# Kernel tuning notes

Hardware: AMD Instinct MI355X
Metric: run time of the kernel (lower is better)

Reference implementation:

```python
import jax, jax.numpy as jnp
import numpy as np

D_MODEL = 512
NUM_HEADS = 8
HEAD_DIM = D_MODEL // NUM_HEADS  # 64
EMBEDDING_DIM = 512  # undefined global EmbeddingDim in source -> d_model
EVENT_DIM = 388      # undefined global EventDim in source -> MIDI event vocab
B, T = 2, 2048


def setup_inputs() -> dict:
    key = jax.random.key(0)
    ks = jax.random.split(key, 12)
    sc = 0.02
    v = jax.random.normal(ks[0], (B, T, D_MODEL), jnp.float32)
    k = jax.random.normal(ks[1], (B, T, D_MODEL), jnp.float32)
    q = jax.random.normal(ks[2], (B, T, D_MODEL), jnp.float32)
    mask = jnp.tril(jnp.ones((T, T), jnp.float32))  # causal mask, broadcasts to [H,B,T,T]
    Wq = jax.random.normal(ks[3], (D_MODEL, HEAD_DIM), jnp.float32) * sc
    bq = jnp.zeros((HEAD_DIM,), jnp.float32)
    Wk = jax.random.normal(ks[4], (D_MODEL, HEAD_DIM), jnp.float32) * sc
    bk = jnp.zeros((HEAD_DIM,), jnp.float32)
    Wv = jax.random.normal(ks[5], (D_MODEL, HEAD_DIM), jnp.float32) * sc
    bv = jnp.zeros((HEAD_DIM,), jnp.float32)
    E = jax.random.normal(ks[6], (NUM_HEADS, T, HEAD_DIM), jnp.float32) * sc
    Wo = jax.random.normal(ks[7], (D_MODEL, EMBEDDING_DIM), jnp.float32) * sc
    bo = jnp.zeros((EMBEDDING_DIM,), jnp.float32)
    Wl = jax.random.normal(ks[8], (EMBEDDING_DIM, EVENT_DIM), jnp.float32) * sc
    bl = jnp.zeros((EVENT_DIM,), jnp.float32)
    return {"v": v, "k": k, "q": q, "mask": mask, "Wq": Wq, "bq": bq,
            "Wk": Wk, "bk": bk, "Wv": Wv, "bv": bv, "E": E,
            "Wo": Wo, "bo": bo, "Wl": Wl, "bl": bl}


def _skew(S):
    # S: [H,B,T,T] -> Music-Transformer skew via left-pad, reshape, slice
    H, Bb, Tt, _ = S.shape
    S = jnp.pad(S, ((0, 0), (0, 0), (0, 0), (1, 0)))          # [H,B,T,T+1]
    S = S.reshape(H, Bb, Tt + 1, Tt)                           # [H,B,T+1,T]
    return S[:, :, 1:]                                         # [H,B,T,T]


def reference(v, k, q, mask, Wq, bq, Wk, bk, Wv, bv, E, Wo, bo, Wl, bl):
    # The source applies the SAME Dense per head, so all heads share q/k/v projections
    qh = q @ Wq + bq  # [B,T,hd]
    kh = k @ Wk + bk  # [B,T,hd]
    vh = v @ Wv + bv  # [B,T,hd]
    # relative-position scores per head: Q @ E^T then skew
    S = jnp.einsum('btd,hsd->hbts', qh, E)  # [H,B,T,T]
    S = _skew(S)
    qk = jnp.einsum('btd,bsd->bts', qh, kh)  # [B,T,T], identical across heads
    attn = (qk[None] + S) / np.sqrt(HEAD_DIM)  # [H,B,T,T]
    attn = attn * mask - jnp.asarray(1e10, attn.dtype) * (1.0 - mask)
    score = jax.nn.softmax(attn, axis=-1)
    ctx = jnp.einsum('hbts,bsd->hbtd', score, vh)  # [H,B,T,hd]
    ctx = jnp.transpose(ctx, (1, 2, 0, 3)).reshape(ctx.shape[1], ctx.shape[2], -1)  # [B,T,d_model]
    ctx = jax.nn.relu(ctx @ Wo + bo)  # [B,T,EmbeddingDim]
    logits = ctx @ Wl + bl            # [B,T,EventDim]
    return logits
```

## Files before the change

kernel.cpp:

```cpp
#include <hip/hip_runtime.h>
#include <hip/hip_bf16.h>


#define B_ 2
#define T_ 2048
#define DM_ 512
#define H_ 8
#define HD_ 64
#define ED_ 512
#define EV_ 388
#define BT_ (B_ * T_)

typedef __attribute__((ext_vector_type(8))) short short8;
typedef __attribute__((ext_vector_type(4))) float floatx4;

#define MFMA(a, b, c) __builtin_amdgcn_mfma_f32_16x16x32_bf16((a), (b), (c), 0, 0, 0)

__device__ __forceinline__ float bfs(unsigned short s) {
  union { unsigned int i; float f; } v; v.i = ((unsigned int)s) << 16; return v.f;
}
__device__ __forceinline__ unsigned short f2bf(float f) {
  __hip_bfloat16 h = __float2bfloat16(f);
  union { __hip_bfloat16 h; unsigned short u; } v; v.h = h; return v.u;
}
__device__ __forceinline__ float ldf(const void* p, int i, bool isbf) {
  return isbf ? bfs(((const unsigned short*)p)[i]) : ((const float*)p)[i];
}
__device__ __forceinline__ bool det_bf(const unsigned int* mask) {
  return mask[0] != 0x3F800000u;
}
__device__ __forceinline__ void gl_lds16(const unsigned short* g, void* l) {
  __builtin_amdgcn_global_load_lds(
      (const __attribute__((address_space(1))) void*)g,
      (__attribute__((address_space(3))) void*)l, 16, 0, 0);
}

__global__ __launch_bounds__(256) void prep_kernel(
    const void* __restrict__ E, const void* __restrict__ Wq,
    const void* __restrict__ Wk, const void* __restrict__ Wv,
    const void* __restrict__ Wo, const void* __restrict__ Wl,
    const unsigned int* __restrict__ mask,
    unsigned short* __restrict__ E_c, unsigned short* __restrict__ WqT,
    unsigned short* __restrict__ WkT, unsigned short* __restrict__ WvT,
    unsigned short* __restrict__ WoT, unsigned short* __restrict__ WlT) {
  const bool isbf = det_bf(mask);
  const int tid = threadIdx.x;
  int bi = blockIdx.x;
  if (bi < 1024) {
    const int i0 = (bi * 256 + tid) * 4;
    if (isbf) {
      *(uint2*)&E_c[i0] = *(const uint2*)((const unsigned short*)E + i0);
    } else {
      float4 f = *(const float4*)((const float*)E + i0);
      unsigned short p[4] = {f2bf(f.x), f2bf(f.y), f2bf(f.z), f2bf(f.w)};
      *(uint2*)&E_c[i0] = *(uint2*)p;
    }
    return;
  }
  bi -= 1024;
  const void* src; unsigned short* dst; int N, nb;
  if (bi < 16)       { src = Wq; dst = WqT; N = 64;  nb = bi; }
  else if (bi < 32)  { src = Wk; dst = WkT; N = 64;  nb = bi - 16; }
  else if (bi < 48)  { src = Wv; dst = WvT; N = 64;  nb = bi - 32; }
  else if (bi < 176) { src = Wo; dst = WoT; N = 512; nb = bi - 48; }
  else               { src = Wl; dst = WlT; N = 388; nb = bi - 176; }
  const int n = nb * 4 + (tid >> 6);
  const int k0 = (tid & 63) * 8;
  unsigned short vv[8];
#pragma unroll
  for (int j = 0; j < 8; ++j) {
    if (n >= N) vv[j] = 0;
    else if (isbf) vv[j] = ((const unsigned short*)src)[(size_t)(k0 + j) * N + n];
    else vv[j] = f2bf(((const float*)src)[(size_t)(k0 + j) * N + n]);
  }
  *(uint4*)&dst[(size_t)n * DM_ + k0] = *(uint4*)vv;
}

__global__ __launch_bounds__(256) void gemm_proj(
    const void* __restrict__ xq, const void* __restrict__ xk,
    const void* __restrict__ xv,
    const unsigned short* __restrict__ WqT, const unsigned short* __restrict__ WkT,
    const unsigned short* __restrict__ WvT,
    const void* __restrict__ bq, const void* __restrict__ bk,
    const void* __restrict__ bv, const unsigned int* __restrict__ mask,
    unsigned short* __restrict__ oq, unsigned short* __restrict__ ok,
    unsigned short* __restrict__ ovt) {
  __shared__ __align__(16) short sA[64][72];
  __shared__ __align__(16) short sW[64][72];
  const int sel = blockIdx.y;
  const void* x = (sel == 0) ? xq : (sel == 1) ? xk : xv;
  const unsigned short* WT = (sel == 0) ? WqT : (sel == 1) ? WkT : WvT;
  const void* bias = (sel == 0) ? bq : (sel == 1) ? bk : bv;
  const bool isbf = det_bf(mask);

  const int tid = threadIdx.x;
  const int w = tid >> 6, lane = tid & 63;
  const int q_ = lane >> 4, n_ = lane & 15;
  const int row0 = blockIdx.x * 64;

  floatx4 acc[4];
#pragma unroll
  for (int j = 0; j < 4; ++j) acc[j] = (floatx4){0.f, 0.f, 0.f, 0.f};

  for (int k0 = 0; k0 < DM_; k0 += 64) {
    if (isbf) {
#pragma unroll
      for (int it = 0; it < 2; ++it) {
        int idx = tid + it * 256;
        int rr = idx >> 3, cc = (idx & 7) * 8;
        *(uint4*)&sA[rr][cc] =
            *(const uint4*)((const unsigned short*)x + (size_t)(row0 + rr) * DM_ + k0 + cc);
      }
    } else {
#pragma unroll
      for (int it = 0; it < 4; ++it) {
        int idx = tid + it * 256;
        int rr = idx >> 4, cc = (idx & 15) * 4;
        float4 f = *(const float4*)((const float*)x + (size_t)(row0 + rr) * DM_ + k0 + cc);
        unsigned short p[4] = {f2bf(f.x), f2bf(f.y), f2bf(f.z), f2bf(f.w)};
        *(uint2*)&sA[rr][cc] = *(uint2*)p;
      }
    }
#pragma unroll
    for (int it = 0; it < 2; ++it) {
      int idx = tid + it * 256;
      int rr = idx >> 3, cc = (idx & 7) * 8;
      *(uint4*)&sW[rr][cc] = *(const uint4*)(WT + (size_t)rr * DM_ + k0 + cc);
    }
    __syncthreads();
    short8 a0 = *(const short8*)&sA[16 * w + n_][8 * q_];
    short8 a1 = *(const short8*)&sA[16 * w + n_][32 + 8 * q_];
#pragma unroll
    for (int nb = 0; nb < 4; ++nb) {
      short8 b0 = *(const short8*)&sW[16 * nb + n_][8 * q_];
      short8 b1 = *(const short8*)&sW[16 * nb + n_][32 + 8 * q_];
      acc[nb] = MFMA(a0, b0, acc[nb]);
      acc[nb] = MFMA(a1, b1, acc[nb]);
    }
    __syncthreads();
  }

#pragma unroll
  for (int nb = 0; nb < 4; ++nb) {
    const int col = 16 * nb + n_;
    const float bb = ldf(bias, col, isbf);
#pragma unroll
    for (int r = 0; r < 4; ++r) {
      int row = row0 + 16 * w + 4 * q_ + r;
      unsigned short val = f2bf(acc[nb][r] + bb);
      if (sel < 2) {
        unsigned short* o = (sel == 0) ? oq : ok;
        o[(size_t)row * HD_ + col] = val;
      } else {
        int b = row >> 11, s = row & 2047;
        ovt[(((size_t)(b * HD_ + col)) << 11) + s] = val;
      }
    }
  }
}

__device__ __forceinline__ int pbase_of(int ti) {
  return (ti < 22) ? (ti - 11) * 2 : 22 + (ti - 22) * 3;
}

__global__ __launch_bounds__(256, 4) void attn_kernel(
    const unsigned short* __restrict__ qh, const unsigned short* __restrict__ kh,
    const unsigned short* __restrict__ vt, const unsigned short* __restrict__ E,
    unsigned short* __restrict__ ctxo, float* __restrict__ pc,
    float* __restrict__ ml) {
  __shared__ __align__(16) short sK[2][64][64];
  __shared__ __align__(16) short sVT[2][64][64];
  __shared__ __align__(16) short sP[64][64];

  const int id = blockIdx.x;
  const int hb = id / 63;
  const int rem = id % 63;
  int ti, c, nc;
  if (rem < 11)      { ti = rem;                  c = 0;              nc = 1; }
  else if (rem < 33) { ti = 11 + ((rem - 11) >> 1); c = (rem - 11) & 1; nc = 2; }
  else               { ti = 22 + (rem - 33) / 3;    c = (rem - 33) % 3; nc = 3; }
  const int nsteps = ti + 1;
  const int klo = (c * nsteps) / nc;
  const int khi = ((c + 1) * nsteps) / nc;

  const int h = hb >> 1, b = hb & 1;
  const int t0 = ti * 64;

  const int tid = threadIdx.x;
  const int w = tid >> 6, lane = tid & 63;
  const int q_ = lane >> 4, n_ = lane & 15;

  const int trow = t0 + 16 * w + n_;
  const unsigned short* qp = qh + (((size_t)((b << 11) + trow)) << 6) + (q_ << 3);
  const short8 qa0 = *(const short8*)qp;
  const short8 qa1 = *(const short8*)(qp + 32);

  short8 onesf;
#pragma unroll
  for (int j = 0; j < 8; ++j) onesf[j] = (short)0x3F80;

  floatx4 ctxa[4];
#pragma unroll
  for (int nb = 0; nb < 4; ++nb) ctxa[nb] = (floatx4){0.f, 0.f, 0.f, 0.f};
  floatx4 lacc = (floatx4){0.f, 0.f, 0.f, 0.f};

  const unsigned short* eb = E + ((size_t)h << 17);
  const unsigned short* kbase = kh + (((size_t)(b << 11)) << 6);
  const unsigned short* vbase = vt + (((size_t)(b << 6)) << 11);

  const int lrow = lane >> 3;
  const int lchunk = ((lane & 7) ^ lrow) << 3;
  const int rK0 = 8 * w + lrow;
  const int c0s = ((q_ ^ (n_ & 7)) << 3);
  const int c1s = (((q_ | 4) ^ (n_ & 7)) << 3);

#define STAGE(bufsel, s0v)                                                     \
  {                                                                            \
    void* dK = (void*)&sK[bufsel][8 * w][0];                                   \
    void* dV = (void*)&sVT[bufsel][8 * w][0];                                  \
    const unsigned short* gK =                                                 \
        kbase + (((size_t)((s0v) + rK0)) << 6) + lchunk;                       \
    const unsigned short* gV =                                                 \
        vbase + (((size_t)rK0) << 11) + (s0v) + lchunk;                        \
    gl_lds16(gK, dK);                                                          \
    gl_lds16(gK + (32 << 6), (void*)((short*)dK + 32 * 64));                   \
    gl_lds16(gV, dV);                                                          \
    gl_lds16(gV + (32 << 11), (void*)((short*)dV + 32 * 64));                  \
  }

  STAGE(0, klo * 64);

  for (int kt = klo; kt < khi; ++kt) {
    const int cur = (kt - klo) & 1;
    const int s0 = kt * 64;

    asm volatile("s_waitcnt vmcnt(0)" ::: "memory");
    __builtin_amdgcn_sched_barrier(0);
    __builtin_amdgcn_s_barrier();
    __builtin_amdgcn_sched_barrier(0);

    if (kt + 1 < khi) STAGE(cur ^ 1, s0 + 64);

    const int rb = (T_ - 64) + s0 - t0;
    short8 e0[5], e1[5];
#pragma unroll
    for (int f = 0; f < 5; ++f) {
      int gr = rb + 16 * (3 - w + f) + n_;
      if (gr > T_ - 1) gr = T_ - 1;
      const unsigned short* ep = eb + ((size_t)gr << 6) + (q_ << 3);
      e0[f] = *(const short8*)ep;
      e1[f] = *(const short8*)(ep + 32);
    }

    floatx4 qk[4];
    __builtin_amdgcn_s_setprio(1);
#pragma unroll
    for (int nb = 0; nb < 4; ++nb) {
      short8 kb0 = *(const short8*)&sK[cur][16 * nb + n_][c0s];
      short8 kb1 = *(const short8*)&sK[cur][16 * nb + n_][c1s];
      qk[nb] = (floatx4){0.f, 0.f, 0.f, 0.f};
      qk[nb] = MFMA(qa0, kb0, qk[nb]);
      qk[nb] = MFMA(qa1, kb1, qk[nb]);
    }
    floatx4 qe[5];
#pragma unroll
    for (int f = 0; f < 5; ++f) {
      qe[f] = (floatx4){0.f, 0.f, 0.f, 0.f};
      qe[f] = MFMA(qa0, e0[f], qe[f]);
      qe[f] = MFMA(qa1, e1[f], qe[f]);
    }
    __builtin_amdgcn_s_setprio(0);

    const bool diag = (kt == ti);
#pragma unroll
    for (int r = 0; r < 4; ++r) {
      const int t = 4 * q_ + r;
      const int ba = ((q_ << 4) | ((n_ - t + 15) & 15)) << 2;
      const int nd = (n_ + t + 1) & 15;
      const bool hi = nd > t;
      const int swr = (t & 7) << 3;
#pragma unroll
      for (int mb = 0; mb < 4; ++mb) {
        float merged = hi ? qe[mb + 1][r] : qe[mb][r];
        float g = __int_as_float(
            __builtin_amdgcn_ds_bpermute(ba, __float_as_int(merged)));
        float sv = qk[mb][r] + g;
        if (diag && (16 * mb + n_ > 16 * w + t)) sv = -1.0e30f;
        sP[16 * w + t][(16 * mb + n_) ^ swr] =
            (short)f2bf(exp2f(sv * 0.18033688011f));
      }
    }

    short8 pa0 = *(const short8*)&sP[16 * w + n_][c0s];
    short8 pa1 = *(const short8*)&sP[16 * w + n_][c1s];
    __builtin_amdgcn_s_setprio(1);
#pragma unroll
    for (int nb = 0; nb < 4; ++nb) {
      short8 v0 = *(const short8*)&sVT[cur][16 * nb + n_][c0s];
      short8 v1 = *(const short8*)&sVT[cur][16 * nb + n_][c1s];
      ctxa[nb] = MFMA(pa0, v0, ctxa[nb]);
      ctxa[nb] = MFMA(pa1, v1, ctxa[nb]);
    }
    lacc = MFMA(pa0, onesf, lacc);
    lacc = MFMA(pa1, onesf, lacc);
    __builtin_amdgcn_s_setprio(0);
  }
#undef STAGE

  if (nc == 1) {
#pragma unroll
    for (int r = 0; r < 4; ++r) {
      const float inv = 1.0f / lacc[r];
      const int row = t0 + 16 * w + 4 * q_ + r;
      const size_t base = (((size_t)((b << 11) + row)) << 9) + (h << 6) + n_;
#pragma unroll
      for (int nb = 0; nb < 4; ++nb)
        ctxo[base + 16 * nb] = f2bf(ctxa[nb][r] * inv);
    }
  } else {
    const int idx = hb * 52 + pbase_of(ti) + c;
    float* pcb = pc + ((size_t)idx << 12);
    float* mlb = ml + ((size_t)idx << 6);
#pragma unroll
    for (int r = 0; r < 4; ++r) {
      const int row = 16 * w + 4 * q_ + r;
#pragma unroll
      for (int nb = 0; nb < 4; ++nb)
        pcb[(row << 6) + 16 * nb + n_] = ctxa[nb][r];
      if (n_ == 0) mlb[row] = lacc[r];
    }
  }
}

__global__ __launch_bounds__(256) void combine_kernel(
    const float* __restrict__ pc, const float* __restrict__ ml,
    unsigned short* __restrict__ ctxo) {
  const int cb = blockIdx.x;
  const int hb = cb / 21;
  const int ti = 11 + cb % 21;
  const int nc = (ti < 22) ? 2 : 3;
  const int h = hb >> 1, b = hb & 1, t0 = ti * 64;
  const int tid = threadIdx.x;
  const int row = tid >> 2, seg = (tid & 3) * 16;
  const int idx0 = hb * 52 + pbase_of(ti);

  float lsum = 0.f;
  float4 a4[4];
#pragma unroll
  for (int j = 0; j < 4; ++j) a4[j] = (float4){0.f, 0.f, 0.f, 0.f};
  for (int c = 0; c < nc; ++c) {
    const int idx = idx0 + c;
    lsum += ml[((size_t)idx << 6) + row];
    const float* cp = pc + ((size_t)idx << 12) + (row << 6) + seg;
#pragma unroll
    for (int j = 0; j < 4; ++j) {
      float4 x = *(const float4*)(cp + 4 * j);
      a4[j].x += x.x; a4[j].y += x.y; a4[j].z += x.z; a4[j].w += x.w;
    }
  }
  const float inv = 1.0f / lsum;
  unsigned short o[16];
#pragma unroll
  for (int j = 0; j < 4; ++j) {
    o[4 * j + 0] = f2bf(a4[j].x * inv);
    o[4 * j + 1] = f2bf(a4[j].y * inv);
    o[4 * j + 2] = f2bf(a4[j].z * inv);
    o[4 * j + 3] = f2bf(a4[j].w * inv);
  }
  unsigned short* dst =
      ctxo + (((size_t)((b << 11) + t0 + row)) << 9) + (h << 6) + seg;
  *(uint4*)dst = *(uint4*)&o[0];
  *(uint4*)(dst + 8) = *(uint4*)&o[8];
}

template <int RELU>
__global__ __launch_bounds__(256) void mlp_mfma(
    const unsigned short* __restrict__ A, const unsigned short* __restrict__ WT,
    const void* __restrict__ bias, unsigned short* __restrict__ outBF,
    void* __restrict__ outD, const unsigned int* __restrict__ mask) {
  __shared__ __align__(16) short sA[64][72];
  __shared__ __align__(16) short sW[64][72];
  const int tid = threadIdx.x;
  const int w = tid >> 6, lane = tid & 63;
  const int q_ = lane >> 4, n_ = lane & 15;
  const int row0 = blockIdx.x * 64;
  const int n0 = blockIdx.y * 64;
  const bool isbf = det_bf(mask);

  floatx4 acc[4];
#pragma unroll
  for (int j = 0; j < 4; ++j) acc[j] = (floatx4){0.f, 0.f, 0.f, 0.f};

  for (int k0 = 0; k0 < DM_; k0 += 64) {
#pragma unroll
    for (int it = 0; it < 2; ++it) {
      int idx = tid + it * 256;
      int rr = idx >> 3, cc = (idx & 7) * 8;
      *(uint4*)&sA[rr][cc] = *(const uint4*)(A + (size_t)(row0 + rr) * DM_ + k0 + cc);
      *(uint4*)&sW[rr][cc] = *(const uint4*)(WT + (size_t)(n0 + rr) * DM_ + k0 + cc);
    }
    __syncthreads();
    short8 a0 = *(const short8*)&sA[16 * w + n_][8 * q_];
    short8 a1 = *(const short8*)&sA[16 * w + n_][32 + 8 * q_];
#pragma unroll
    for (int nb = 0; nb < 4; ++nb) {
      short8 b0 = *(const short8*)&sW[16 * nb + n_][8 * q_];
      short8 b1 = *(const short8*)&sW[16 * nb + n_][32 + 8 * q_];
      acc[nb] = MFMA(a0, b0, acc[nb]);
      acc[nb] = MFMA(a1, b1, acc[nb]);
    }
    __syncthreads();
  }

#pragma unroll
  for (int nb = 0; nb < 4; ++nb) {
    const int col = n0 + 16 * nb + n_;
    float bb = 0.f;
    if (RELU || col < EV_) bb = ldf(bias, col, isbf);
#pragma unroll
    for (int r = 0; r < 4; ++r) {
      const int row = row0 + 16 * w + 4 * q_ + r;
      float v = acc[nb][r] + bb;
      if (RELU) {
        outBF[(size_t)row * ED_ + col] = f2bf(fmaxf(v, 0.f));
      } else if (col < EV_) {
        if (isbf) ((unsigned short*)outD)[(size_t)row * EV_ + col] = f2bf(v);
        else      ((float*)outD)[(size_t)row * EV_ + col] = v;
      }
    }
  }
}

extern "C" void kernel_launch(void* const* d_in, const int* in_sizes, int n_in,
                              void* d_out, int out_size, void* d_ws, size_t ws_size,
                              hipStream_t stream) {
  const void* v  = d_in[0];
  const void* k  = d_in[1];
  const void* q  = d_in[2];
  const unsigned int* mask = (const unsigned int*)d_in[3];
  const void* Wq = d_in[4];
  const void* bq = d_in[5];
  const void* Wk = d_in[6];
  const void* bk = d_in[7];
  const void* Wv = d_in[8];
  const void* bv = d_in[9];
  const void* E  = d_in[10];
  const void* Wo = d_in[11];
  const void* bo = d_in[12];
  const void* Wl = d_in[13];
  const void* bl = d_in[14];

  char* p = (char*)d_ws;
  unsigned short* E_c  = (unsigned short*)p; p += (size_t)H_ * T_ * HD_ * 2;
  unsigned short* qhb  = (unsigned short*)p; p += (size_t)BT_ * HD_ * 2;
  unsigned short* khb  = (unsigned short*)p; p += (size_t)BT_ * HD_ * 2;
  unsigned short* vtb  = (unsigned short*)p; p += (size_t)BT_ * HD_ * 2;
  unsigned short* WqT  = (unsigned short*)p; p += (size_t)HD_ * DM_ * 2;
  unsigned short* WkT  = (unsigned short*)p; p += (size_t)HD_ * DM_ * 2;
  unsigned short* WvT  = (unsigned short*)p; p += (size_t)HD_ * DM_ * 2;
  unsigned short* WoT  = (unsigned short*)p; p += (size_t)ED_ * DM_ * 2;
  unsigned short* WlT  = (unsigned short*)p; p += (size_t)448 * DM_ * 2;
  unsigned short* ctxb = (unsigned short*)p; p += (size_t)BT_ * DM_ * 2;
  unsigned short* h1b  = (unsigned short*)p; p += (size_t)BT_ * ED_ * 2;
  float* pc = (float*)p; p += (size_t)16 * 52 * 4096 * 4;
  float* ml = (float*)p; p += (size_t)16 * 52 * 64 * 4;

  prep_kernel<<<dim3(1312), 256, 0, stream>>>(
      E, Wq, Wk, Wv, Wo, Wl, mask, E_c, WqT, WkT, WvT, WoT, WlT);
  gemm_proj<<<dim3(BT_ / 64, 3), 256, 0, stream>>>(
      q, k, v, WqT, WkT, WvT, bq, bk, bv, mask, qhb, khb, vtb);
  attn_kernel<<<dim3(1008), 256, 0, stream>>>(qhb, khb, vtb, E_c, ctxb, pc, ml);
  combine_kernel<<<dim3(336), 256, 0, stream>>>(pc, ml, ctxb);
  mlp_mfma<1><<<dim3(BT_ / 64, ED_ / 64), 256, 0, stream>>>(
      ctxb, WoT, bo, h1b, nullptr, mask);
  mlp_mfma<0><<<dim3(BT_ / 64, 448 / 64), 256, 0, stream>>>(
      h1b, WlT, bl, nullptr, d_out, mask);
}
```

Measured before the change: 217.9 us.

## Halve attention KV tile to 32 and split causal rows into more chunks

After: 310.4 us. +42.4%, slower.

```diff
diff --git a/kernel.cpp b/kernel.cpp
--- a/kernel.cpp
+++ b/kernel.cpp
@@ -160,26 +160,33 @@
 }
 
 __device__ __forceinline__ int pbase_of(int ti) {
-  return (ti < 22) ? (ti - 11) * 2 : 22 + (ti - 22) * 3;
-}
-
-__global__ __launch_bounds__(256, 4) void attn_kernel(
+  return (ti < 11) ? (ti - 5) * 2
+       : (ti < 16) ? 12 + (ti - 11) * 3
+       : (ti < 22) ? 27 + (ti - 16) * 4
+       : (ti < 27) ? 51 + (ti - 22) * 5
+                   : 76 + (ti - 27) * 6;
+}
+
+__global__ __launch_bounds__(256, 8) void attn_kernel(
     const unsigned short* __restrict__ qh, const unsigned short* __restrict__ kh,
     const unsigned short* __restrict__ vt, const unsigned short* __restrict__ E,
     unsigned short* __restrict__ ctxo, float* __restrict__ pc,
     float* __restrict__ ml) {
-  __shared__ __align__(16) short sK[2][64][64];
-  __shared__ __align__(16) short sVT[2][64][64];
-  __shared__ __align__(16) short sP[64][64];
+  __shared__ __align__(16) short sK[2][32][64];
+  __shared__ __align__(16) short sVT[2][64][32];
+  __shared__ __align__(16) short sP[64][32];
 
   const int id = blockIdx.x;
-  const int hb = id / 63;
-  const int rem = id % 63;
+  const int hb = id / 111;
+  const int rem = id % 111;
   int ti, c, nc;
-  if (rem < 11)      { ti = rem;                  c = 0;              nc = 1; }
-  else if (rem < 33) { ti = 11 + ((rem - 11) >> 1); c = (rem - 11) & 1; nc = 2; }
-  else               { ti = 22 + (rem - 33) / 3;    c = (rem - 33) % 3; nc = 3; }
-  const int nsteps = ti + 1;
+  if (rem < 5)       { ti = rem;                  c = 0;              nc = 1; }
+  else if (rem < 17) { ti = 5 + (rem - 5) / 2;    c = (rem - 5) % 2;  nc = 2; }
+  else if (rem < 32) { ti = 11 + (rem - 17) / 3;  c = (rem - 17) % 3; nc = 3; }
+  else if (rem < 56) { ti = 16 + (rem - 32) / 4;  c = (rem - 32) % 4; nc = 4; }
+  else if (rem < 81) { ti = 22 + (rem - 56) / 5;  c = (rem - 56) % 5; nc = 5; }
+  else               { ti = 27 + (rem - 81) / 6;  c = (rem - 81) % 6; nc = 6; }
+  const int nsteps = 2 * (ti + 1);
   const int klo = (c * nsteps) / nc;
   const int khi = ((c + 1) * nsteps) / nc;
 
@@ -208,101 +215,96 @@
   const unsigned short* kbase = kh + (((size_t)(b << 11)) << 6);
   const unsigned short* vbase = vt + (((size_t)(b << 6)) << 11);
 
-  const int lrow = lane >> 3;
-  const int lchunk = ((lane & 7) ^ lrow) << 3;
-  const int rK0 = 8 * w + lrow;
+  const int kRow = lane >> 3;
+  const int kChk = ((lane & 7) ^ kRow) << 3;
+  const int vRow = lane >> 2;
+  const int vChk = ((lane & 3) ^ (vRow & 3)) << 3;
   const int c0s = ((q_ ^ (n_ & 7)) << 3);
   const int c1s = (((q_ | 4) ^ (n_ & 7)) << 3);
+  const int cv  = ((q_ ^ (n_ & 3)) << 3);
 
 #define STAGE(bufsel, s0v)                                                     \
   {                                                                            \
-    void* dK = (void*)&sK[bufsel][8 * w][0];                                   \
-    void* dV = (void*)&sVT[bufsel][8 * w][0];                                  \
     const unsigned short* gK =                                                 \
-        kbase + (((size_t)((s0v) + rK0)) << 6) + lchunk;                       \
+        kbase + (((size_t)((s0v) + 8 * w + kRow)) << 6) + kChk;                \
     const unsigned short* gV =                                                 \
-        vbase + (((size_t)rK0) << 11) + (s0v) + lchunk;                        \
-    gl_lds16(gK, dK);                                                          \
-    gl_lds16(gK + (32 << 6), (void*)((short*)dK + 32 * 64));                   \
-    gl_lds16(gV, dV);                                                          \
-    gl_lds16(gV + (32 << 11), (void*)((short*)dV + 32 * 64));                  \
-  }
-
-  STAGE(0, klo * 64);
+        vbase + (((size_t)(16 * w + vRow)) << 11) + (s0v) + vChk;              \
+    gl_lds16(gK, (void*)&sK[bufsel][8 * w][0]);                                \
+    gl_lds16(gV, (void*)&sVT[bufsel][16 * w][0]);                              \
+  }
+
+  STAGE(0, klo * 32);
 
   for (int kt = klo; kt < khi; ++kt) {
     const int cur = (kt - klo) & 1;
-    const int s0 = kt * 64;
+    const int s0 = kt * 32;
 
     asm volatile("s_waitcnt vmcnt(0)" ::: "memory");
     __builtin_amdgcn_sched_barrier(0);
     __builtin_amdgcn_s_barrier();
     __builtin_amdgcn_sched_barrier(0);
 
-    if (kt + 1 < khi) STAGE(cur ^ 1, s0 + 64);
+    if (kt + 1 < khi) STAGE(cur ^ 1, s0 + 32);
 
     const int rb = (T_ - 64) + s0 - t0;
-    short8 e0[5], e1[5];
-#pragma unroll
-    for (int f = 0; f < 5; ++f) {
-      int gr = rb + 16 * (3 - w + f) + n_;
+    short8 e0[3], e1[3];
+#pragma unroll
+    for (int f = 0; f < 3; ++f) {
+      int gr = rb + 48 - 16 * w + 16 * f + n_;
       if (gr > T_ - 1) gr = T_ - 1;
       const unsigned short* ep = eb + ((size_t)gr << 6) + (q_ << 3);
       e0[f] = *(const short8*)ep;
       e1[f] = *(const short8*)(ep + 32);
     }
 
-    floatx4 qk[4];
+    floatx4 qk[2];
     __builtin_amdgcn_s_setprio(1);
 #pragma unroll
-    for (int nb = 0; nb < 4; ++nb) {
-      short8 kb0 = *(const short8*)&sK[cur][16 * nb + n_][c0s];
-      short8 kb1 = *(const short8*)&sK[cur][16 * nb + n_][c1s];
-      qk[nb] = (floatx4){0.f, 0.f, 0.f, 0.f};
-      qk[nb] = MFMA(qa0, kb0, qk[nb]);
-      qk[nb] = MFMA(qa1, kb1, qk[nb]);
-    }
-    floatx4 qe[5];
-#pragma unroll
-    for (int f = 0; f < 5; ++f) {
+    for (int mb = 0; mb < 2; ++mb) {
+      short8 kb0 = *(const short8*)&sK[cur][16 * mb + n_][c0s];
+      short8 kb1 = *(const short8*)&sK[cur][16 * mb + n_][c1s];
+      qk[mb] = (floatx4){0.f, 0.f, 0.f, 0.f};
+      qk[mb] = MFMA(qa0, kb0, qk[mb]);
+      qk[mb] = MFMA(qa1, kb1, qk[mb]);
+    }
+    floatx4 qe[3];
+#pragma unroll
+    for (int f = 0; f < 3; ++f) {
       qe[f] = (floatx4){0.f, 0.f, 0.f, 0.f};
       qe[f] = MFMA(qa0, e0[f], qe[f]);
       qe[f] = MFMA(qa1, e1[f], qe[f]);
     }
     __builtin_amdgcn_s_setprio(0);
 
-    const bool diag = (kt == ti);
+    const int sd = s0 - t0;
 #pragma unroll
     for (int r = 0; r < 4; ++r) {
       const int t = 4 * q_ + r;
       const int ba = ((q_ << 4) | ((n_ - t + 15) & 15)) << 2;
       const int nd = (n_ + t + 1) & 15;
       const bool hi = nd > t;
-      const int swr = (t & 7) << 3;
-#pragma unroll
-      for (int mb = 0; mb < 4; ++mb) {
+      const int thr = 16 * w + t - sd;
+      const int swr = (t & 3) << 3;
+#pragma unroll
+      for (int mb = 0; mb < 2; ++mb) {
         float merged = hi ? qe[mb + 1][r] : qe[mb][r];
         float g = __int_as_float(
             __builtin_amdgcn_ds_bpermute(ba, __float_as_int(merged)));
         float sv = qk[mb][r] + g;
-        if (diag && (16 * mb + n_ > 16 * w + t)) sv = -1.0e30f;
+        if (16 * mb + n_ > thr) sv = -1.0e30f;
         sP[16 * w + t][(16 * mb + n_) ^ swr] =
             (short)f2bf(exp2f(sv * 0.18033688011f));
       }
     }
 
-    short8 pa0 = *(const short8*)&sP[16 * w + n_][c0s];
-    short8 pa1 = *(const short8*)&sP[16 * w + n_][c1s];
+    short8 pa0 = *(const short8*)&sP[16 * w + n_][cv];
     __builtin_amdgcn_s_setprio(1);
 #pragma unroll
     for (int nb = 0; nb < 4; ++nb) {
-      short8 v0 = *(const short8*)&sVT[cur][16 * nb + n_][c0s];
-      short8 v1 = *(const short8*)&sVT[cur][16 * nb + n_][c1s];
+      short8 v0 = *(const short8*)&sVT[cur][16 * nb + n_][cv];
       ctxa[nb] = MFMA(pa0, v0, ctxa[nb]);
-      ctxa[nb] = MFMA(pa1, v1, ctxa[nb]);
     }
     lacc = MFMA(pa0, onesf, lacc);
-    lacc = MFMA(pa1, onesf, lacc);
     __builtin_amdgcn_s_setprio(0);
   }
 #undef STAGE
@@ -318,7 +320,7 @@
         ctxo[base + 16 * nb] = f2bf(ctxa[nb][r] * inv);
     }
   } else {
-    const int idx = hb * 52 + pbase_of(ti) + c;
+    const int idx = hb * 106 + pbase_of(ti) + c;
     float* pcb = pc + ((size_t)idx << 12);
     float* mlb = ml + ((size_t)idx << 6);
 #pragma unroll
@@ -336,13 +338,14 @@
     const float* __restrict__ pc, const float* __restrict__ ml,
     unsigned short* __restrict__ ctxo) {
   const int cb = blockIdx.x;
-  const int hb = cb / 21;
-  const int ti = 11 + cb % 21;
-  const int nc = (ti < 22) ? 2 : 3;
+  const int hb = cb / 27;
+  const int ti = 5 + cb % 27;
+  const int nc = (ti < 11) ? 2 : (ti < 16) ? 3 : (ti < 22) ? 4
+               : (ti < 27) ? 5 : 6;
   const int h = hb >> 1, b = hb & 1, t0 = ti * 64;
   const int tid = threadIdx.x;
   const int row = tid >> 2, seg = (tid & 3) * 16;
-  const int idx0 = hb * 52 + pbase_of(ti);
+  const int idx0 = hb * 106 + pbase_of(ti);
 
   float lsum = 0.f;
   float4 a4[4];
@@ -462,15 +465,15 @@
   unsigned short* WlT  = (unsigned short*)p; p += (size_t)448 * DM_ * 2;
   unsigned short* ctxb = (unsigned short*)p; p += (size_t)BT_ * DM_ * 2;
   unsigned short* h1b  = (unsigned short*)p; p += (size_t)BT_ * ED_ * 2;
-  float* pc = (float*)p; p += (size_t)16 * 52 * 4096 * 4;
-  float* ml = (float*)p; p += (size_t)16 * 52 * 64 * 4;
+  float* pc = (float*)p; p += (size_t)16 * 106 * 4096 * 4;
+  float* ml = (float*)p; p += (size_t)16 * 106 * 64 * 4;
 
   prep_kernel<<<dim3(1312), 256, 0, stream>>>(
       E, Wq, Wk, Wv, Wo, Wl, mask, E_c, WqT, WkT, WvT, WoT, WlT);
   gemm_proj<<<dim3(BT_ / 64, 3), 256, 0, stream>>>(
       q, k, v, WqT, WkT, WvT, bq, bk, bv, mask, qhb, khb, vtb);
-  attn_kernel<<<dim3(1008), 256, 0, stream>>>(qhb, khb, vtb, E_c, ctxb, pc, ml);
-  combine_kernel<<<dim3(336), 256, 0, stream>>>(pc, ml, ctxb);
+  attn_kernel<<<dim3(1776), 256, 0, stream>>>(qhb, khb, vtb, E_c, ctxb, pc, ml);
+  combine_kernel<<<dim3(432), 256, 0, stream>>>(pc, ml, ctxb);
   mlp_mfma<1><<<dim3(BT_ / 64, ED_ / 64), 256, 0, stream>>>(
       ctxb, WoT, bo, h1b, nullptr, mask);
   mlp_mfma<0><<<dim3(BT_ / 64, 448 / 64), 256, 0, stream>>>(
```
